# Kernel optimization log

Measured on AMD Instinct MI355X. Metric: run time of the kernel, lower is better.

The kernel has to match this reference:

```python
import jax, jax.numpy as jnp
import numpy as np

B, IN_C, IN_L, T = 8, 64, 64, 256
OUT_C, OUT_L = 64, 64
KH, KW = 3, 3
K = IN_C * KH * KW  # 576
EPS = 1e-5


def setup_inputs() -> dict:
    key = jax.random.key(0)
    k1, k2 = jax.random.split(key, 2)
    x = jax.random.normal(k1, (B, IN_C, IN_L, T), dtype=jnp.float32)
    # xavier-normal-ish scale for fan_in = K
    weight = jax.random.normal(k2, (K, OUT_C, OUT_L), dtype=jnp.float32) * (1.0 / np.sqrt(K))
    bias = jnp.zeros((OUT_C, OUT_L), dtype=jnp.float32)
    gamma = jnp.ones((OUT_C,), dtype=jnp.float32)
    beta = jnp.zeros((OUT_C,), dtype=jnp.float32)
    alpha = jnp.full((1,), 0.25, dtype=jnp.float32)  # PReLU single-parameter init
    return {"x": x, "weight": weight, "bias": bias, "gamma": gamma, "beta": beta, "alpha": alpha}


def _unfold3x3(x):
    # torch nn.Unfold(kernel=(3,3), stride=1, padding=1): output channel index = c*9 + i*3 + j
    xp = jnp.pad(x, ((0, 0), (0, 0), (1, 1), (1, 1)))
    pats = jnp.stack([xp[:, :, i:i + IN_L, j:j + T] for i in range(KH) for j in range(KW)], axis=2)  # (B, C, 9, L, T)
    return pats.reshape(x.shape[0], K, IN_L, T)


def reference(x, weight, bias, gamma, beta, alpha):
    patches = _unfold3x3(x)  # (B, K, L, T); out_l_unfold == in_l, out_t == t, so slicing is a no-op
    # locally-connected conv: per out_l position weight, shared over time
    out = jnp.einsum('bklt,kcl->bclt', patches, weight)  # (B, out_c, out_l, T)
    out = out + bias[None, :, :, None]
    # BatchNorm2d (training mode: batch statistics, biased variance)
    mean = out.mean(axis=(0, 2, 3), keepdims=True)
    var = out.var(axis=(0, 2, 3), keepdims=True)
    out = (out - mean) * jax.lax.rsqrt(var + EPS) * gamma[None, :, None, None] + beta[None, :, None, None]
    # PReLU with single shared parameter
    return jnp.where(out >= 0, out, alpha[0] * out)
```

## Files before the change

kernel.cpp:

```cpp
#include <hip/hip_runtime.h>

typedef __attribute__((ext_vector_type(8))) short short8;
typedef __attribute__((ext_vector_type(8))) unsigned short ushort8;
typedef __attribute__((ext_vector_type(4))) float f32x4;

constexpr int B_ = 8, IN_C_ = 64, IN_L_ = 64, T_ = 256, OUT_C_ = 64, OUT_L_ = 64;
constexpr float EPS_ = 1e-5f;

constexpr int XT_LP = 66, XT_TP = 258, XT_IC = 64;
constexpr int XT_LSTRIDE = XT_TP * XT_IC;
constexpr int XT_BSTRIDE = XT_LP * XT_LSTRIDE;
constexpr size_t XT_ELEMS = (size_t)B_ * XT_BSTRIDE;
constexpr size_t XT_BYTES = XT_ELEMS * 2;
constexpr size_t WT2_ELEMS = 64ull * 9 * 64 * 64;
constexpr size_t WT2_OFF_B = XT_BYTES;
constexpr size_t PART_OFF_B = WT2_OFF_B + WT2_ELEMS * 2;
constexpr size_t SS_OFF_B = PART_OFF_B + 512ull * 128 * 4;
constexpr size_t WS_NEED = SS_OFF_B + 128 * 4;
constexpr size_t TMP_OFF_B = WS_NEED;
constexpr size_t TMP_BYTES = (size_t)B_ * OUT_C_ * OUT_L_ * T_ * 2;
constexpr size_t WS_NEED2 = TMP_OFF_B + TMP_BYTES;

__device__ __forceinline__ unsigned short f2bf(float f) {
  unsigned u = __float_as_uint(f);
  return (unsigned short)((u + 0x7fffu + ((u >> 16) & 1u)) >> 16);
}

__device__ __forceinline__ void gload_lds16(const void* g, void* l) {
  __builtin_amdgcn_global_load_lds(
      (const __attribute__((address_space(1))) unsigned int*)g,
      (__attribute__((address_space(3))) unsigned int*)l, 16, 0, 0);
}

__global__ __launch_bounds__(256) void prep_kernel(const float* __restrict__ x,
                                                   const float* __restrict__ w,
                                                   unsigned short* __restrict__ xT,
                                                   unsigned short* __restrict__ wT2) {
  const int bid = blockIdx.x;
  const int tid = threadIdx.x;
  __shared__ unsigned char shmem[34816];
  if (bid < 144) {
    const int tap = bid >> 4;
    const int c0 = (bid & 15) * 4;
    auto wls = (unsigned short(*)[4][68])shmem;
    {
      const int ic = tid >> 2, cl = tid & 3;
      const float* src = w + (((size_t)(ic * 9 + tap) * 64) + (c0 + cl)) * 64;
#pragma unroll
      for (int e = 0; e < 16; ++e) {
        float4 v = ((const float4*)src)[e];
        const int l = e * 4;
        wls[l + 0][cl][ic] = f2bf(v.x);
        wls[l + 1][cl][ic] = f2bf(v.y);
        wls[l + 2][cl][ic] = f2bf(v.z);
        wls[l + 3][cl][ic] = f2bf(v.w);
      }
    }
    __syncthreads();
    {
      const int l = tid >> 2, cl = tid & 3;
      const unsigned short* row = &wls[l][cl][0];
      uint4* dst = (uint4*)(wT2 + ((size_t)(l * 9 + tap)) * 4096 + (c0 + cl) * 64);
#pragma unroll
      for (int q = 0; q < 8; ++q) dst[q] = ((const uint4*)row)[q];
    }
  } else if (bid < 1168) {
    const int u = bid - 144;
    const int th = u & 1, l = (u >> 1) & 63, b = u >> 7;
    const int t0 = th * 128;
    auto ls = (unsigned short(*)[132])shmem;
    {
      const int ic = tid >> 2, q = tid & 3;
      const float4* src = (const float4*)(x + (((size_t)(b * 64 + ic) * 64 + l) * 256 + t0));
#pragma unroll
      for (int e = 0; e < 8; ++e) {
        float4 v = src[q * 8 + e];
        const int toff = (q * 8 + e) * 4;
        unsigned d0 = f2bf(v.x) | ((unsigned)f2bf(v.y) << 16);
        unsigned d1 = f2bf(v.z) | ((unsigned)f2bf(v.w) << 16);
        *(uint2*)&ls[ic][toff] = make_uint2(d0, d1);
      }
    }
    __syncthreads();
    {
      const int tl = tid >> 1, h = tid & 1;
      unsigned d[16];
#pragma unroll
      for (int k = 0; k < 16; ++k) {
        unsigned short a = ls[h * 32 + 2 * k][tl];
        unsigned short c = ls[h * 32 + 2 * k + 1][tl];
        d[k] = a | ((unsigned)c << 16);
      }
      unsigned short* dst =
          xT + ((size_t)(b * XT_LP + l + 1) * XT_TP + (t0 + tl + 1)) * XT_IC + h * 32;
      uint4* dv = (uint4*)dst;
      dv[0] = make_uint4(d[0], d[1], d[2], d[3]);
      dv[1] = make_uint4(d[4], d[5], d[6], d[7]);
      dv[2] = make_uint4(d[8], d[9], d[10], d[11]);
      dv[3] = make_uint4(d[12], d[13], d[14], d[15]);
    }
  } else {
    const int b = bid - 1168;
    unsigned short* base = xT + (size_t)b * XT_BSTRIDE;
    const short8 z = {};
    for (int ci = tid; ci < 5184; ci += 256) {
      size_t off;
      if (ci < 4128) {
        const int plane = ci / 2064, k = ci % 2064;
        off = (size_t)(plane ? 65 : 0) * XT_LSTRIDE + (size_t)k * 8;
      } else {
        const int k = ci - 4128;
        const int lp = k >> 4, rem = k & 15;
        const int tp = (rem < 8) ? 0 : 257;
        off = ((size_t)lp * XT_TP + tp) * 64 + (size_t)(rem & 7) * 8;
      }
      *(short8*)(base + off) = z;
    }
  }
}

__global__ __launch_bounds__(256, 2) void conv_mfma(
    const unsigned short* __restrict__ xT, const unsigned short* __restrict__ wT2,
    const float* __restrict__ bias, float* __restrict__ outf,
    unsigned short* __restrict__ tmpb, float* __restrict__ part) {
  const int orig = blockIdx.x;
  const int wg = (orig >> 6) * 64 + (orig & 7) * 8 + ((orig >> 3) & 7);
  const int b = wg >> 6, l = wg & 63;
  const int tid = threadIdx.x;
  const int wid = tid >> 6, ln = tid & 63;
  const int lc = ln & 15, lg = ln >> 4;
  const int m0 = wid * 64;

  __shared__ unsigned short lds[2][20480];

  const int src_lane_off = ((ln >> 3) << 6) + ((((ln & 7) ^ (ln >> 3))) << 3);
  const unsigned short* xBase = xT + (size_t)(b * XT_LP + l) * XT_LSTRIDE + src_lane_off;
  const unsigned short* wBase = wT2 + (size_t)l * 9 * 4096 + src_lane_off;

  auto STAGE = [&](int buf, int tap) {
    const int i = tap / 3, j = tap - i * 3;
    const unsigned short* Ab = xBase + (size_t)i * XT_LSTRIDE + j * 64;
    unsigned short* La = &lds[buf][0];
#pragma unroll
    for (int q = 0; q < 8; ++q) {
      const int ch = wid * 8 + q;
      gload_lds16(Ab + ch * 512, La + ch * 512);
    }
    const unsigned short* Bb = wBase + (size_t)tap * 4096;
    unsigned short* Lb = &lds[buf][16384];
#pragma unroll
    for (int q = 0; q < 2; ++q) {
      const int ch = wid * 2 + q;
      gload_lds16(Bb + ch * 512, Lb + ch * 512);
    }
  };

  f32x4 acc[4][4] = {};

  STAGE(0, 0);
#pragma unroll
  for (int tap = 0; tap < 9; ++tap) {
    __builtin_amdgcn_s_barrier();
    if (tap + 1 < 9) {
      STAGE((tap + 1) & 1, tap + 1);
      asm volatile("s_waitcnt vmcnt(10)" ::: "memory");
    } else {
      asm volatile("s_waitcnt vmcnt(0)" ::: "memory");
    }
    __builtin_amdgcn_sched_barrier(0);
    __builtin_amdgcn_s_barrier();
    __builtin_amdgcn_sched_barrier(0);

    const unsigned short* La = &lds[tap & 1][0];
    const unsigned short* Lb = &lds[tap & 1][16384];
#pragma unroll
    for (int kb = 0; kb < 2; ++kb) {
      const int slot = (((kb * 4 + lg) ^ (lc & 7)) << 3);
      short8 af[4], bf[4];
#pragma unroll
      for (int mi = 0; mi < 4; ++mi)
        af[mi] = *(const short8*)(La + (m0 + mi * 16 + lc) * 64 + slot);
#pragma unroll
      for (int ni = 0; ni < 4; ++ni)
        bf[ni] = *(const short8*)(Lb + (ni * 16 + lc) * 64 + slot);
#pragma unroll
      for (int mi = 0; mi < 4; ++mi)
#pragma unroll
        for (int ni = 0; ni < 4; ++ni)
          acc[mi][ni] =
              __builtin_amdgcn_mfma_f32_16x16x32_bf16(af[mi], bf[ni], acc[mi][ni], 0, 0, 0);
    }
  }

  __syncthreads();
  float* sm = (float*)&lds[0][0];
#pragma unroll
  for (int ni = 0; ni < 4; ++ni) {
    const int c = ni * 16 + lc;
    const float bv = bias[c * 64 + l];
    float s = 0.f, s2 = 0.f;
    const size_t obase = ((size_t)(b * 64 + c) * 64 + l) * 256 + m0;
#pragma unroll
    for (int mi = 0; mi < 4; ++mi) {
      float vv[4];
#pragma unroll
      for (int r = 0; r < 4; ++r) {
        float v = acc[mi][ni][r] + bv;
        vv[r] = v;
        s += v;
        s2 += v * v;
      }
      if (tmpb) {
        unsigned d0 = f2bf(vv[0]) | ((unsigned)f2bf(vv[1]) << 16);
        unsigned d1 = f2bf(vv[2]) | ((unsigned)f2bf(vv[3]) << 16);
        *(uint2*)(tmpb + obase + mi * 16 + lg * 4) = make_uint2(d0, d1);
      } else {
        *(float4*)(outf + obase + mi * 16 + lg * 4) =
            make_float4(vv[0], vv[1], vv[2], vv[3]);
      }
    }
    s += __shfl_xor(s, 16);  s += __shfl_xor(s, 32);
    s2 += __shfl_xor(s2, 16); s2 += __shfl_xor(s2, 32);
    if (lg == 0) {
      sm[(wid * 4 + ni) * 32 + lc * 2] = s;
      sm[(wid * 4 + ni) * 32 + lc * 2 + 1] = s2;
    }
  }
  __syncthreads();
  if (tid < 128) {
    const int sel = tid >> 6, cc = tid & 63;
    const int ni = cc >> 4, lc2 = cc & 15;
    float r = 0.f;
#pragma unroll
    for (int w2 = 0; w2 < 4; ++w2) r += sm[(w2 * 4 + ni) * 32 + lc2 * 2 + sel];
    part[(size_t)wg * 128 + sel * 64 + cc] = r;
  }
}

__global__ __launch_bounds__(256) void stats_final_mf(
    const float* __restrict__ part, const float* __restrict__ gamma,
    const float* __restrict__ beta, float* __restrict__ ss) {
  const int c = blockIdx.x;
  const int tid = threadIdx.x;
  float s = 0.f, s2 = 0.f;
  for (int blk = tid; blk < 512; blk += 256) {
    s += part[(size_t)blk * 128 + c];
    s2 += part[(size_t)blk * 128 + 64 + c];
  }
#pragma unroll
  for (int off = 32; off; off >>= 1) {
    s += __shfl_down(s, off);
    s2 += __shfl_down(s2, off);
  }
  __shared__ float r0[4], r1[4];
  const int wid = tid >> 6, lane = tid & 63;
  if (lane == 0) { r0[wid] = s; r1[wid] = s2; }
  __syncthreads();
  if (tid == 0) {
    float S = r0[0] + r0[1] + r0[2] + r0[3];
    float S2 = r1[0] + r1[1] + r1[2] + r1[3];
    const float inv_n = 1.0f / 131072.f;
    float mean = S * inv_n;
    float var = S2 * inv_n - mean * mean;
    float inv = rsqrtf(var + EPS_);
    float sc = gamma[c] * inv;
    ss[c] = sc;
    ss[64 + c] = beta[c] - mean * sc;
  }
}

__global__ __launch_bounds__(256) void bn_prelu_b(
    const unsigned short* __restrict__ tmp, const float* __restrict__ ss,
    const float* __restrict__ alpha, float* __restrict__ out) {
  const float a = alpha[0];
  constexpr size_t N8 = (size_t)B_ * OUT_C_ * OUT_L_ * T_ / 8;
  for (size_t i = (size_t)blockIdx.x * 256 + threadIdx.x; i < N8;
       i += (size_t)gridDim.x * 256) {
    const int c = (int)((i >> 11) & 63);
    const float sc = ss[c];
    const float sh = ss[64 + c];
    ushort8 v = *(const ushort8*)(tmp + i * 8);
    float o[8];
#pragma unroll
    for (int r = 0; r < 8; ++r) {
      float f = __uint_as_float(((unsigned)v[r]) << 16) * sc + sh;
      o[r] = (f >= 0.f) ? f : a * f;
    }
    float4* op = (float4*)(out + i * 8);
    op[0] = make_float4(o[0], o[1], o[2], o[3]);
    op[1] = make_float4(o[4], o[5], o[6], o[7]);
  }
}

__global__ __launch_bounds__(256) void bn_prelu(
    float* __restrict__ out, const float* __restrict__ scaleshift,
    const float* __restrict__ alpha) {
  const float a = alpha[0];
  constexpr size_t N4 = (size_t)B_ * OUT_C_ * OUT_L_ * T_ / 4;
  float4* p = (float4*)out;
  for (size_t i = (size_t)blockIdx.x * 256 + threadIdx.x; i < N4;
       i += (size_t)gridDim.x * 256) {
    const int c = (int)((i >> 12) & 63);
    const float sc = scaleshift[c];
    const float sh = scaleshift[64 + c];
    float4 v = p[i];
    v.x = v.x * sc + sh; v.x = (v.x >= 0.f) ? v.x : a * v.x;
    v.y = v.y * sc + sh; v.y = (v.y >= 0.f) ? v.y : a * v.y;
    v.z = v.z * sc + sh; v.z = (v.z >= 0.f) ? v.z : a * v.z;
    v.w = v.w * sc + sh; v.w = (v.w >= 0.f) ? v.w : a * v.w;
    p[i] = v;
  }
}

extern "C" void kernel_launch(void* const* d_in, const int* in_sizes, int n_in,
                              void* d_out, int out_size, void* d_ws, size_t ws_size,
                              hipStream_t stream) {
  const float* x = (const float*)d_in[0];
  const float* w = (const float*)d_in[1];
  const float* bias = (const float*)d_in[2];
  const float* gamma = (const float*)d_in[3];
  const float* beta = (const float*)d_in[4];
  const float* alpha = (const float*)d_in[5];
  float* out = (float*)d_out;

  unsigned short* xT = (unsigned short*)d_ws;
  unsigned short* wT2 = (unsigned short*)((char*)d_ws + WT2_OFF_B);
  float* part = (float*)((char*)d_ws + PART_OFF_B);
  float* ssb = (float*)((char*)d_ws + SS_OFF_B);

  if (ws_size >= WS_NEED2) {
    unsigned short* tmpb = (unsigned short*)((char*)d_ws + TMP_OFF_B);
    prep_kernel<<<dim3(1176), dim3(256), 0, stream>>>(x, w, xT, wT2);
    conv_mfma<<<dim3(512), dim3(256), 0, stream>>>(xT, wT2, bias, out, tmpb, part);
    stats_final_mf<<<dim3(64), dim3(256), 0, stream>>>(part, gamma, beta, ssb);
    bn_prelu_b<<<dim3(2048), dim3(256), 0, stream>>>(tmpb, ssb, alpha, out);
  } else if (ws_size >= WS_NEED) {
    prep_kernel<<<dim3(1176), dim3(256), 0, stream>>>(x, w, xT, wT2);
    conv_mfma<<<dim3(512), dim3(256), 0, stream>>>(xT, wT2, bias, out, nullptr, part);
    stats_final_mf<<<dim3(64), dim3(256), 0, stream>>>(part, gamma, beta, ssb);
    bn_prelu<<<dim3(2048), dim3(256), 0, stream>>>(out, ssb, alpha);
  }
}
```

Measured before the change: 51.69 us.

## Split conv tiles along time, stage input once in LDS, fuse stats into BN

The conv kernel now splits each (batch, l) tile into two 128-wide time halves, giving 1024 blocks instead of 512. Each block loads the whole 3-row by 130-column input window into LDS once with a swizzled layout. The 9 taps then read shifted slices of that window, so only the weights are double-buffered per tap, which cuts input reloads. The separate statistics-finalize kernel is folded into the BN+PReLU kernel: every block redundantly reduces the 1024 partial sums for its channel, removing one launch but adding redundant reads of the partials.

```diff
diff --git a/kernel.cpp b/kernel.cpp
--- a/kernel.cpp
+++ b/kernel.cpp
@@ -15,10 +15,10 @@
 constexpr size_t WT2_ELEMS = 64ull * 9 * 64 * 64;
 constexpr size_t WT2_OFF_B = XT_BYTES;
 constexpr size_t PART_OFF_B = WT2_OFF_B + WT2_ELEMS * 2;
-constexpr size_t SS_OFF_B = PART_OFF_B + 512ull * 128 * 4;
-constexpr size_t WS_NEED = SS_OFF_B + 128 * 4;
-constexpr size_t TMP_OFF_B = WS_NEED;
+constexpr size_t PART_BYTES = 1024ull * 128 * 4;
+constexpr size_t TMP_OFF_B = PART_OFF_B + PART_BYTES;
 constexpr size_t TMP_BYTES = (size_t)B_ * OUT_C_ * OUT_L_ * T_ * 2;
+constexpr size_t WS_NEED = TMP_OFF_B;
 constexpr size_t WS_NEED2 = TMP_OFF_B + TMP_BYTES;
 
 __device__ __forceinline__ unsigned short f2bf(float f) {
@@ -124,46 +124,57 @@
     const float* __restrict__ bias, float* __restrict__ outf,
     unsigned short* __restrict__ tmpb, float* __restrict__ part) {
   const int orig = blockIdx.x;
-  const int wg = (orig >> 6) * 64 + (orig & 7) * 8 + ((orig >> 3) & 7);
-  const int b = wg >> 6, l = wg & 63;
+  const int xcd = orig & 7;
+  const int idx = orig >> 3;
+  const int b = idx >> 4;
+  const int th = (idx >> 3) & 1;
+  const int l = xcd * 8 + (idx & 7);
+  const int wg = ((b << 6) + l) * 2 + th;
   const int tid = threadIdx.x;
   const int wid = tid >> 6, ln = tid & 63;
   const int lc = ln & 15, lg = ln >> 4;
-  const int m0 = wid * 64;
-
-  __shared__ unsigned short lds[2][20480];
-
-  const int src_lane_off = ((ln >> 3) << 6) + ((((ln & 7) ^ (ln >> 3))) << 3);
-  const unsigned short* xBase = xT + (size_t)(b * XT_LP + l) * XT_LSTRIDE + src_lane_off;
-  const unsigned short* wBase = wT2 + (size_t)l * 9 * 4096 + src_lane_off;
-
-  auto STAGE = [&](int buf, int tap) {
-    const int i = tap / 3, j = tap - i * 3;
-    const unsigned short* Ab = xBase + (size_t)i * XT_LSTRIDE + j * 64;
-    unsigned short* La = &lds[buf][0];
-#pragma unroll
-    for (int q = 0; q < 8; ++q) {
-      const int ch = wid * 8 + q;
-      gload_lds16(Ab + ch * 512, La + ch * 512);
-    }
-    const unsigned short* Bb = wBase + (size_t)tap * 4096;
-    unsigned short* Lb = &lds[buf][16384];
+  const int m0 = wid * 32;
+  const int tp0 = th * 128;
+
+  __shared__ unsigned short Al[26624];
+  __shared__ unsigned short Bl[2][4096];
+
+  {
+    const unsigned short* rbase = xT + ((size_t)(b * XT_LP + l) * XT_TP + tp0) * 64;
+#pragma unroll
+    for (int k = 0; k < 13; ++k) {
+      const int cbase = k * 256 + wid * 64;
+      const int ci = cbase + ln;
+      const int i = ci / 1040;
+      const int r = ci - i * 1040;
+      const int d = r >> 3, s = r & 7;
+      gload_lds16(rbase + (size_t)i * XT_LSTRIDE + d * 64 + ((s ^ (d & 7)) << 3),
+                  Al + (size_t)cbase * 8);
+    }
+  }
+  const unsigned short* wBase = wT2 + (size_t)l * 9 * 4096;
+  auto BSTAGE = [&](int buf, int tap) {
 #pragma unroll
     for (int q = 0; q < 2; ++q) {
-      const int ch = wid * 2 + q;
-      gload_lds16(Bb + ch * 512, Lb + ch * 512);
+      const int cbase = q * 256 + wid * 64;
+      const int ci = cbase + ln;
+      const int crow = ci >> 3, s = ci & 7;
+      gload_lds16(wBase + (size_t)tap * 4096 + crow * 64 + ((s ^ (crow & 7)) << 3),
+                  &Bl[buf][0] + (size_t)cbase * 8);
     }
   };
 
-  f32x4 acc[4][4] = {};
-
-  STAGE(0, 0);
+  f32x4 acc[2][4] = {};
+
+  BSTAGE(0, 0);
+  __syncthreads();
+
 #pragma unroll
   for (int tap = 0; tap < 9; ++tap) {
     __builtin_amdgcn_s_barrier();
     if (tap + 1 < 9) {
-      STAGE((tap + 1) & 1, tap + 1);
-      asm volatile("s_waitcnt vmcnt(10)" ::: "memory");
+      BSTAGE((tap + 1) & 1, tap + 1);
+      asm volatile("s_waitcnt vmcnt(2)" ::: "memory");
     } else {
       asm volatile("s_waitcnt vmcnt(0)" ::: "memory");
     }
@@ -171,20 +182,23 @@
     __builtin_amdgcn_s_barrier();
     __builtin_amdgcn_sched_barrier(0);
 
-    const unsigned short* La = &lds[tap & 1][0];
-    const unsigned short* Lb = &lds[tap & 1][16384];
+    const int i = tap / 3, j = tap - (tap / 3) * 3;
+    const unsigned short* Lb = &Bl[tap & 1][0];
 #pragma unroll
     for (int kb = 0; kb < 2; ++kb) {
-      const int slot = (((kb * 4 + lg) ^ (lc & 7)) << 3);
-      short8 af[4], bf[4];
-#pragma unroll
-      for (int mi = 0; mi < 4; ++mi)
-        af[mi] = *(const short8*)(La + (m0 + mi * 16 + lc) * 64 + slot);
+      short8 af[2], bf[4];
+#pragma unroll
+      for (int mi = 0; mi < 2; ++mi) {
+        const int d = m0 + mi * 16 + lc + j;
+        af[mi] = *(const short8*)(Al + (i * 130 + d) * 64 +
+                                  (((kb * 4 + lg) ^ (d & 7)) << 3));
+      }
 #pragma unroll
       for (int ni = 0; ni < 4; ++ni)
-        bf[ni] = *(const short8*)(Lb + (ni * 16 + lc) * 64 + slot);
-#pragma unroll
-      for (int mi = 0; mi < 4; ++mi)
+        bf[ni] = *(const short8*)(Lb + (ni * 16 + lc) * 64 +
+                                  (((kb * 4 + lg) ^ (lc & 7)) << 3));
+#pragma unroll
+      for (int mi = 0; mi < 2; ++mi)
 #pragma unroll
         for (int ni = 0; ni < 4; ++ni)
           acc[mi][ni] =
@@ -193,15 +207,15 @@
   }
 
   __syncthreads();
-  float* sm = (float*)&lds[0][0];
+  float* sm = (float*)&Al[0];
 #pragma unroll
   for (int ni = 0; ni < 4; ++ni) {
     const int c = ni * 16 + lc;
     const float bv = bias[c * 64 + l];
     float s = 0.f, s2 = 0.f;
-    const size_t obase = ((size_t)(b * 64 + c) * 64 + l) * 256 + m0;
-#pragma unroll
-    for (int mi = 0; mi < 4; ++mi) {
+    const size_t obase = ((size_t)(b * 64 + c) * 64 + l) * 256 + tp0 + m0;
+#pragma unroll
+    for (int mi = 0; mi < 2; ++mi) {
       float vv[4];
 #pragma unroll
       for (int r = 0; r < 4; ++r) {
@@ -237,15 +251,17 @@
   }
 }
 
-__global__ __launch_bounds__(256) void stats_final_mf(
+__global__ __launch_bounds__(256) void bn_stats_prelu_b(
     const float* __restrict__ part, const float* __restrict__ gamma,
-    const float* __restrict__ beta, float* __restrict__ ss) {
-  const int c = blockIdx.x;
+    const float* __restrict__ beta, const float* __restrict__ alpha,
+    const unsigned short* __restrict__ tmp, float* __restrict__ out) {
+  const int c = blockIdx.x >> 5;
+  const int seg = blockIdx.x & 31;
   const int tid = threadIdx.x;
   float s = 0.f, s2 = 0.f;
-  for (int blk = tid; blk < 512; blk += 256) {
-    s += part[(size_t)blk * 128 + c];
-    s2 += part[(size_t)blk * 128 + 64 + c];
+  for (int i = tid; i < 1024; i += 256) {
+    s += part[(size_t)i * 128 + c];
+    s2 += part[(size_t)i * 128 + 64 + c];
   }
 #pragma unroll
   for (int off = 32; off; off >>= 1) {
@@ -256,29 +272,18 @@
   const int wid = tid >> 6, lane = tid & 63;
   if (lane == 0) { r0[wid] = s; r1[wid] = s2; }
   __syncthreads();
-  if (tid == 0) {
-    float S = r0[0] + r0[1] + r0[2] + r0[3];
-    float S2 = r1[0] + r1[1] + r1[2] + r1[3];
-    const float inv_n = 1.0f / 131072.f;
-    float mean = S * inv_n;
-    float var = S2 * inv_n - mean * mean;
-    float inv = rsqrtf(var + EPS_);
-    float sc = gamma[c] * inv;
-    ss[c] = sc;
-    ss[64 + c] = beta[c] - mean * sc;
-  }
-}
-
-__global__ __launch_bounds__(256) void bn_prelu_b(
-    const unsigned short* __restrict__ tmp, const float* __restrict__ ss,
-    const float* __restrict__ alpha, float* __restrict__ out) {
+  const float S = r0[0] + r0[1] + r0[2] + r0[3];
+  const float S2 = r1[0] + r1[1] + r1[2] + r1[3];
+  const float inv_n = 1.0f / 131072.f;
+  const float mean = S * inv_n;
+  const float var = S2 * inv_n - mean * mean;
+  const float sc = gamma[c] * rsqrtf(var + EPS_);
+  const float sh = beta[c] - mean * sc;
   const float a = alpha[0];
-  constexpr size_t N8 = (size_t)B_ * OUT_C_ * OUT_L_ * T_ / 8;
-  for (size_t i = (size_t)blockIdx.x * 256 + threadIdx.x; i < N8;
-       i += (size_t)gridDim.x * 256) {
-    const int c = (int)((i >> 11) & 63);
-    const float sc = ss[c];
-    const float sh = ss[64 + c];
+  const size_t base8 = ((size_t)((seg >> 2) * 64 + c)) * 2048 + (size_t)(seg & 3) * 512;
+#pragma unroll 2
+  for (int k = tid; k < 512; k += 256) {
+    const size_t i = base8 + k;
     ushort8 v = *(const ushort8*)(tmp + i * 8);
     float o[8];
 #pragma unroll
@@ -292,23 +297,43 @@
   }
 }
 
-__global__ __launch_bounds__(256) void bn_prelu(
-    float* __restrict__ out, const float* __restrict__ scaleshift,
-    const float* __restrict__ alpha) {
+__global__ __launch_bounds__(256) void bn_stats_prelu_f(
+    const float* __restrict__ part, const float* __restrict__ gamma,
+    const float* __restrict__ beta, const float* __restrict__ alpha,
+    float* __restrict__ out) {
+  const int c = blockIdx.x >> 5;
+  const int seg = blockIdx.x & 31;
+  const int tid = threadIdx.x;
+  float s = 0.f, s2 = 0.f;
+  for (int i = tid; i < 1024; i += 256) {
+    s += part[(size_t)i * 128 + c];
+    s2 += part[(size_t)i * 128 + 64 + c];
+  }
+#pragma unroll
+  for (int off = 32; off; off >>= 1) {
+    s += __shfl_down(s, off);
+    s2 += __shfl_down(s2, off);
+  }
+  __shared__ float r0[4], r1[4];
+  const int wid = tid >> 6, lane = tid & 63;
+  if (lane == 0) { r0[wid] = s; r1[wid] = s2; }
+  __syncthreads();
+  const float S = r0[0] + r0[1] + r0[2] + r0[3];
+  const float S2 = r1[0] + r1[1] + r1[2] + r1[3];
+  const float inv_n = 1.0f / 131072.f;
+  const float mean = S * inv_n;
+  const float var = S2 * inv_n - mean * mean;
+  const float sc = gamma[c] * rsqrtf(var + EPS_);
+  const float sh = beta[c] - mean * sc;
   const float a = alpha[0];
-  constexpr size_t N4 = (size_t)B_ * OUT_C_ * OUT_L_ * T_ / 4;
-  float4* p = (float4*)out;
-  for (size_t i = (size_t)blockIdx.x * 256 + threadIdx.x; i < N4;
-       i += (size_t)gridDim.x * 256) {
-    const int c = (int)((i >> 12) & 63);
-    const float sc = scaleshift[c];
-    const float sh = scaleshift[64 + c];
-    float4 v = p[i];
+  const size_t base4 = ((size_t)((seg >> 2) * 64 + c)) * 4096 + (size_t)(seg & 3) * 1024;
+  for (int k = tid; k < 1024; k += 256) {
+    float4 v = ((float4*)out)[base4 + k];
     v.x = v.x * sc + sh; v.x = (v.x >= 0.f) ? v.x : a * v.x;
     v.y = v.y * sc + sh; v.y = (v.y >= 0.f) ? v.y : a * v.y;
     v.z = v.z * sc + sh; v.z = (v.z >= 0.f) ? v.z : a * v.z;
     v.w = v.w * sc + sh; v.w = (v.w >= 0.f) ? v.w : a * v.w;
-    p[i] = v;
+    ((float4*)out)[base4 + k] = v;
   }
 }
 
@@ -326,18 +351,15 @@
   unsigned short* xT = (unsigned short*)d_ws;
   unsigned short* wT2 = (unsigned short*)((char*)d_ws + WT2_OFF_B);
   float* part = (float*)((char*)d_ws + PART_OFF_B);
-  float* ssb = (float*)((char*)d_ws + SS_OFF_B);
 
   if (ws_size >= WS_NEED2) {
     unsigned short* tmpb = (unsigned short*)((char*)d_ws + TMP_OFF_B);
     prep_kernel<<<dim3(1176), dim3(256), 0, stream>>>(x, w, xT, wT2);
-    conv_mfma<<<dim3(512), dim3(256), 0, stream>>>(xT, wT2, bias, out, tmpb, part);
-    stats_final_mf<<<dim3(64), dim3(256), 0, stream>>>(part, gamma, beta, ssb);
-    bn_prelu_b<<<dim3(2048), dim3(256), 0, stream>>>(tmpb, ssb, alpha, out);
+    conv_mfma<<<dim3(1024), dim3(256), 0, stream>>>(xT, wT2, bias, out, tmpb, part);
+    bn_stats_prelu_b<<<dim3(2048), dim3(256), 0, stream>>>(part, gamma, beta, alpha, tmpb, out);
   } else if (ws_size >= WS_NEED) {
     prep_kernel<<<dim3(1176), dim3(256), 0, stream>>>(x, w, xT, wT2);
-    conv_mfma<<<dim3(512), dim3(256), 0, stream>>>(xT, wT2, bias, out, nullptr, part);
-    stats_final_mf<<<dim3(64), dim3(256), 0, stream>>>(part, gamma, beta, ssb);
-    bn_prelu<<<dim3(2048), dim3(256), 0, stream>>>(out, ssb, alpha);
-  }
-}
+    conv_mfma<<<dim3(1024), dim3(256), 0, stream>>>(xT, wT2, bias, out, nullptr, part);
+    bn_stats_prelu_f<<<dim3(2048), dim3(256), 0, stream>>>(part, gamma, beta, alpha, out);
+  }
+}
```

Result: slower. 61.30 us (+18.6%).
